# Performance work log

Measured on AMD Instinct MI355X. Metric: run time of the kernel, lower is better.

The kernel has to match this reference:

```python
import jax, jax.numpy as jnp
import numpy as np

CH = 256
NH = 8
HD = CH // NH  # 32


def setup_inputs() -> dict:
    key = jax.random.key(0)
    k1, k2, k3, k4 = jax.random.split(key, 4)
    x = jax.random.normal(k1, (2, CH, 16, 16, 16), dtype=jnp.float32)
    # 1x1x1 Conv3d weights == per-voxel linear maps over channels
    qkv_w = jax.random.normal(k2, (3 * CH, CH), dtype=jnp.float32) * (1.0 / np.sqrt(CH))
    proj_w = jax.random.normal(k3, (CH, CH), dtype=jnp.float32) * (1.0 / np.sqrt(CH))
    proj_b = jax.random.normal(k4, (CH,), dtype=jnp.float32) * 0.01
    return {"x": x, "qkv_w": qkv_w, "proj_w": proj_w, "proj_b": proj_b}


def reference(x, qkv_w, proj_w, proj_b):
    B, C, D, H, W = x.shape
    N = D * H * W
    nh, hd = NH, HD
    xf = x.reshape(B, C, N)  # [B, C, N]
    # qkv 1x1x1 conv: [B, 3C, N]
    qkv = jnp.einsum('oc,bcn->bon', qkv_w, xf)
    # split channel dim as (3, nh, hd), then arrange to [3, B, nh, N, hd]
    qkv = qkv.reshape(B, 3, nh, hd, N).transpose(1, 0, 2, 4, 3)
    q, k, v = qkv[0], qkv[1], qkv[2]
    scale = hd ** -0.5
    attn = jnp.einsum('bhqd,bhkd->bhqk', q, k) * scale  # [B, nh, N, N]
    attn = jax.nn.softmax(attn, axis=-1)
    # dropout is identity in eval mode
    out = jnp.einsum('bhqk,bhkd->bhqd', attn, v)  # [B, nh, N, hd]
    out = out.transpose(0, 1, 3, 2).reshape(B, C, D, H, W)
    out = jnp.einsum('oc,bcdhw->bodhw', proj_w, out) + proj_b[None, :, None, None, None]
    return out
```

## Files before the change

kernel.cpp:

```cpp
#include <hip/hip_runtime.h>
#include <hip/hip_bf16.h>

typedef __bf16 bf16;
typedef __bf16 bf16x8 __attribute__((ext_vector_type(8)));
typedef float f32x4 __attribute__((ext_vector_type(4)));
typedef float f32x16 __attribute__((ext_vector_type(16)));
typedef unsigned int u32x4 __attribute__((ext_vector_type(4)));

#define EXP2(x) __builtin_amdgcn_exp2f(x)

static __device__ __forceinline__ f32x4 mfma16(bf16x8 a, bf16x8 b, f32x4 c) {
    return __builtin_amdgcn_mfma_f32_16x16x32_bf16(a, b, c, 0, 0, 0);
}
static __device__ __forceinline__ f32x16 mfma32(bf16x8 a, bf16x8 b, f32x16 c) {
    return __builtin_amdgcn_mfma_f32_32x32x16_bf16(a, b, c, 0, 0, 0);
}
static __device__ __forceinline__ unsigned cvt_pk(float lo, float hi) {
    unsigned r;
    asm("v_cvt_pk_bf16_f32 %0, %1, %2" : "=v"(r) : "v"(lo), "v"(hi));
    return r;
}
static __device__ __forceinline__ void perm32swap(unsigned &a, unsigned &b) {
    asm("v_permlane32_swap_b32 %0, %1" : "+v"(a), "+v"(b));
}

__global__ __launch_bounds__(256) void prep_w_kernel(const float* __restrict__ qkv_w,
                                                     const float* __restrict__ proj_w,
                                                     bf16* __restrict__ wqkv,
                                                     bf16* __restrict__ wproj) {
    int idx = blockIdx.x * 256 + threadIdx.x;
    const float QSCALE = 0.17677669529663689f * 1.4426950408889634f;
    if (idx < 768 * 256) {
        float v = qkv_w[idx];
        if (idx < 256 * 256) v *= QSCALE;
        wqkv[idx] = (bf16)v;
    } else {
        int j = idx - 768 * 256;
        wproj[j] = (bf16)proj_w[j];
    }
}

__global__ __launch_bounds__(256) void transpose_x_kernel(const float* __restrict__ x,
                                                          bf16* __restrict__ xT) {
    __shared__ float tile[64][68];
    int b = blockIdx.z, cb = blockIdx.y * 64, nb = blockIdx.x * 64;
    int t = threadIdx.x;
    int j = t & 15, rc = t >> 4;
    const float* src = x + ((size_t)b * 256 + cb) * 4096 + nb;
#pragma unroll
    for (int i = 0; i < 4; i++) {
        f32x4 v = *(const f32x4*)(src + (size_t)(rc + i * 16) * 4096 + j * 4);
        *(f32x4*)&tile[rc + i * 16][j * 4] = v;
    }
    __syncthreads();
    int n = t >> 2;
    bf16* dst = xT + ((size_t)b * 4096 + nb + n) * 256 + cb;
#pragma unroll
    for (int i = 0; i < 2; i++) {
        int c0 = ((t & 3) + i * 4) * 8;
        bf16x8 v;
#pragma unroll
        for (int jj = 0; jj < 8; jj++) v[jj] = (bf16)tile[c0 + jj][n];
        *(bf16x8*)(dst + c0) = v;
    }
}

__global__ __launch_bounds__(256) void qkv_gemm_kernel(const bf16* __restrict__ xT,
                                                       const bf16* __restrict__ w,
                                                       bf16* __restrict__ Q,
                                                       bf16* __restrict__ Kp,
                                                       bf16* __restrict__ Vp) {
    int b = blockIdx.z;
    int nb = blockIdx.x * 64, ob = blockIdx.y * 128;
    int t = threadIdx.x, wid = t >> 6, lane = t & 63;
    int l15 = lane & 15, g = lane >> 4;
    int wr = wid >> 1, wc = wid & 1;
    const bf16* xrow = xT + ((size_t)b * 4096 + nb + wr * 32 + l15) * 256 + g * 8;
    const bf16* wrow = w + (size_t)(ob + wc * 64 + l15) * 256 + g * 8;
    f32x4 acc[2][4] = {};
    for (int k0 = 0; k0 < 256; k0 += 32) {
        bf16x8 a[2], bb[4];
#pragma unroll
        for (int rt = 0; rt < 2; rt++) a[rt] = *(const bf16x8*)(xrow + rt * 16 * 256 + k0);
#pragma unroll
        for (int cg = 0; cg < 4; cg++) bb[cg] = *(const bf16x8*)(wrow + cg * 16 * 256 + k0);
#pragma unroll
        for (int rt = 0; rt < 2; rt++)
#pragma unroll
            for (int cg = 0; cg < 4; cg++)
                acc[rt][cg] = mfma16(a[rt], bb[cg], acc[rt][cg]);
    }
#pragma unroll
    for (int rt = 0; rt < 2; rt++) {
#pragma unroll
        for (int cg = 0; cg < 4; cg++) {
            int o = ob + wc * 64 + cg * 16 + l15;
            int tsel = o >> 8;
            int h = (o >> 5) & 7;
            int d = o & 31;
            int n0 = nb + wr * 32 + rt * 16 + g * 4;
            size_t bhbase = ((size_t)b * 8 + h) * 131072;
            if (tsel == 0) {
#pragma unroll
                for (int i = 0; i < 4; i++)
                    Q[(((size_t)b * 8 + h) * 4096 + n0 + i) * 32 + d] = (bf16)acc[rt][cg][i];
            } else if (tsel == 1) {
                int kt = n0 >> 5;
                int which = d >> 4, hi2 = (d >> 3) & 1, j = d & 7;
                size_t base = bhbase + (size_t)(((kt * 2 + which) * 64 + hi2 * 32) * 8 + j);
#pragma unroll
                for (int i = 0; i < 4; i++) {
                    int r5 = (n0 + i) & 31;
                    Kp[base + r5 * 8] = (bf16)acc[rt][cg][i];
                }
            } else {
                int kt = n0 >> 5, kk0 = n0 & 31;
                int which = kk0 >> 4, hi2 = (kk0 >> 3) & 1, j0 = kk0 & 7;
                unsigned p0 = cvt_pk(acc[rt][cg][0], acc[rt][cg][1]);
                unsigned p1 = cvt_pk(acc[rt][cg][2], acc[rt][cg][3]);
                uint2 wv; wv.x = p0; wv.y = p1;
                *(uint2*)(Vp + bhbase + (size_t)(((kt * 2 + which) * 64 + hi2 * 32 + d) * 8 + j0)) = wv;
            }
        }
    }
}

#define PACK(stv, B, OUT) {                                  \
    unsigned _x01 = cvt_pk(stv[B + 0], stv[B + 1]);          \
    unsigned _x23 = cvt_pk(stv[B + 2], stv[B + 3]);          \
    unsigned _y01 = cvt_pk(stv[B + 4], stv[B + 5]);          \
    unsigned _y23 = cvt_pk(stv[B + 6], stv[B + 7]);          \
    perm32swap(_x01, _y01);                                  \
    perm32swap(_x23, _y23);                                  \
    u32x4 _w = {_x01, _x23, _y01, _y23};                     \
    OUT = __builtin_bit_cast(bf16x8, _w); }

__global__ __launch_bounds__(512, 6) void attn_kernel(const bf16* __restrict__ Q,
                                                      const bf16* __restrict__ Kp,
                                                      const bf16* __restrict__ Vp,
                                                      bf16* __restrict__ attT) {
    __shared__ __align__(16) float ldsO[3][2][64][20];
    __shared__ float ldsL[3][2][32];

    const int w = blockIdx.x;
    const int bh = (w & 7) + 8 * ((w >> 3) & 1);
    const int qblk = w >> 4;
    const int t = threadIdx.x;
    const int wid = t >> 6, lane = t & 63;
    const int z = wid >> 1, wq = wid & 1;
    const int l31 = lane & 31, hi = lane >> 5;
    const int q0 = qblk * 64 + wq * 32;

    const bf16* __restrict__ Qb = Q + (size_t)bh * 4096 * 32;
    const bf16* kptr = Kp + (size_t)bh * 131072 + (size_t)z * 32768 + lane * 8;
    const bf16* vptr = Vp + (size_t)bh * 131072 + (size_t)z * 32768 + lane * 8;

    bf16x8 qf0 = *(const bf16x8*)(Qb + (size_t)(q0 + l31) * 32 + hi * 8);
    bf16x8 qf1 = *(const bf16x8*)(Qb + (size_t)(q0 + l31) * 32 + 16 + hi * 8);

    const f32x16 ZERO16 = {};
    f32x16 o_acc = {};
    float lpart = 0.f;

    for (int it = 0; it < 32; ++it) {
        bf16x8 kf0 = *(const bf16x8*)(kptr);
        bf16x8 kf1 = *(const bf16x8*)(kptr + 512);
        bf16x8 vf0 = *(const bf16x8*)(vptr);
        bf16x8 vf1 = *(const bf16x8*)(vptr + 512);
        kptr += 1024; vptr += 1024;

        f32x16 st = mfma32(kf0, qf0, ZERO16);
        st = mfma32(kf1, qf1, st);

#pragma unroll
        for (int r = 0; r < 16; r++) st[r] = EXP2(st[r]);

        float s0 = 0.f, s1 = 0.f;
#pragma unroll
        for (int r = 0; r < 8; r++) { s0 += st[r]; s1 += st[r + 8]; }
        lpart += s0 + s1;

        bf16x8 pb0, pb1;
        PACK(st, 0, pb0);
        PACK(st, 8, pb1);

        __builtin_amdgcn_s_setprio(1);
        o_acc = mfma32(vf0, pb0, o_acc);
        o_acc = mfma32(vf1, pb1, o_acc);
        __builtin_amdgcn_s_setprio(0);
    }

    lpart += __shfl_xor(lpart, 32);

    if (z != 0) {
#pragma unroll
        for (int g = 0; g < 4; g++) {
            f32x4 wv = {o_acc[4 * g + 0], o_acc[4 * g + 1], o_acc[4 * g + 2], o_acc[4 * g + 3]};
            *(f32x4*)&ldsO[z - 1][wq][lane][4 * g] = wv;
        }
        if (hi == 0) ldsL[z - 1][wq][l31] = lpart;
    }
    __syncthreads();
    if (z == 0) {
        float lsum = lpart + ldsL[0][wq][l31] + ldsL[1][wq][l31] + ldsL[2][wq][l31];
        float inv = __builtin_amdgcn_rcpf(lsum);
        const int b = bh >> 3, h = bh & 7;
        bf16* orow = attT + ((size_t)b * 4096 + q0 + l31) * 256 + h * 32 + 4 * hi;
#pragma unroll
        for (int g = 0; g < 4; g++) {
            f32x4 p0 = *(const f32x4*)&ldsO[0][wq][lane][4 * g];
            f32x4 p1 = *(const f32x4*)&ldsO[1][wq][lane][4 * g];
            f32x4 p2 = *(const f32x4*)&ldsO[2][wq][lane][4 * g];
            float e0 = (o_acc[4 * g + 0] + p0[0] + p1[0] + p2[0]) * inv;
            float e1 = (o_acc[4 * g + 1] + p0[1] + p1[1] + p2[1]) * inv;
            float e2 = (o_acc[4 * g + 2] + p0[2] + p1[2] + p2[2]) * inv;
            float e3 = (o_acc[4 * g + 3] + p0[3] + p1[3] + p2[3]) * inv;
            uint2 wv;
            wv.x = cvt_pk(e0, e1);
            wv.y = cvt_pk(e2, e3);
            *(uint2*)(orow + 8 * g) = wv;
        }
    }
}

__global__ __launch_bounds__(256) void proj_gemm_kernel(const bf16* __restrict__ attT,
                                                        const bf16* __restrict__ w,
                                                        const float* __restrict__ bias,
                                                        float* __restrict__ out) {
    int b = blockIdx.z;
    int nb = blockIdx.x * 64, ob = blockIdx.y * 64;
    int t = threadIdx.x, wid = t >> 6, lane = t & 63;
    int l15 = lane & 15, g = lane >> 4;
    int wr = wid >> 1, wc = wid & 1;
    const bf16* arow = w + (size_t)(ob + wr * 32 + l15) * 256 + g * 8;
    const bf16* brow = attT + ((size_t)b * 4096 + nb + wc * 32 + l15) * 256 + g * 8;
    f32x4 acc[2][2] = {};
    for (int k0 = 0; k0 < 256; k0 += 32) {
        bf16x8 a[2], bb[2];
#pragma unroll
        for (int rt = 0; rt < 2; rt++) a[rt] = *(const bf16x8*)(arow + rt * 16 * 256 + k0);
#pragma unroll
        for (int cg = 0; cg < 2; cg++) bb[cg] = *(const bf16x8*)(brow + cg * 16 * 256 + k0);
#pragma unroll
        for (int rt = 0; rt < 2; rt++)
#pragma unroll
            for (int cg = 0; cg < 2; cg++)
                acc[rt][cg] = mfma16(a[rt], bb[cg], acc[rt][cg]);
    }
#pragma unroll
    for (int rt = 0; rt < 2; rt++)
#pragma unroll
        for (int cg = 0; cg < 2; cg++)
#pragma unroll
            for (int i = 0; i < 4; i++) {
                int o = ob + wr * 32 + rt * 16 + g * 4 + i;
                int n = nb + wc * 32 + cg * 16 + l15;
                out[((size_t)b * 256 + o) * 4096 + n] = acc[rt][cg][i] + bias[o];
            }
}

extern "C" void kernel_launch(void* const* d_in, const int* in_sizes, int n_in,
                              void* d_out, int out_size, void* d_ws, size_t ws_size,
                              hipStream_t stream) {
    const float* x      = (const float*)d_in[0];
    const float* qkv_w  = (const float*)d_in[1];
    const float* proj_w = (const float*)d_in[2];
    const float* proj_b = (const float*)d_in[3];
    float* out = (float*)d_out;

    char* ws = (char*)d_ws;
    bf16* xT    = (bf16*)(ws);
    bf16* wqkv  = (bf16*)(ws + 4194304);
    bf16* wproj = (bf16*)(ws + 4587520);
    bf16* Qb    = (bf16*)(ws + 4718592);
    bf16* Kp    = (bf16*)(ws + 8912896);
    bf16* Vp    = (bf16*)(ws + 13107200);
    bf16* attT  = (bf16*)(ws + 17301504);

    prep_w_kernel<<<1024, 256, 0, stream>>>(qkv_w, proj_w, wqkv, wproj);
    transpose_x_kernel<<<dim3(64, 4, 2), 256, 0, stream>>>(x, xT);
    qkv_gemm_kernel<<<dim3(64, 6, 2), 256, 0, stream>>>(xT, wqkv, Qb, Kp, Vp);
    attn_kernel<<<1024, 512, 0, stream>>>(Qb, Kp, Vp, attT);
    proj_gemm_kernel<<<dim3(64, 4, 2), 256, 0, stream>>>(attT, wproj, proj_b, out);
}
```

Measured before the change: 96.48 us.

## Share K/V loads across two query tiles per wave and pre-pack proj operands

The attention kernel now uses 256 threads, and each wave handles two 32-row query tiles. Each wave reuses the K and V fragments it loads for both tiles, halving global K/V traffic per query and doubling the work per wave. The attention output and the projection weight are now written in an MFMA-fragment-packed layout, so the projection GEMM uses 32x32x16 MFMAs with contiguous coalesced fragment loads. The trade-offs are more registers per wave (two accumulators) and the loss of the launch-bounds occupancy hint, which may reduce occupancy and latency hiding.

```diff
diff --git a/kernel.cpp b/kernel.cpp
--- a/kernel.cpp
+++ b/kernel.cpp
@@ -27,7 +27,7 @@
 __global__ __launch_bounds__(256) void prep_w_kernel(const float* __restrict__ qkv_w,
                                                      const float* __restrict__ proj_w,
                                                      bf16* __restrict__ wqkv,
-                                                     bf16* __restrict__ wproj) {
+                                                     bf16* __restrict__ Wp) {
     int idx = blockIdx.x * 256 + threadIdx.x;
     const float QSCALE = 0.17677669529663689f * 1.4426950408889634f;
     if (idx < 768 * 256) {
@@ -36,7 +36,10 @@
         wqkv[idx] = (bf16)v;
     } else {
         int j = idx - 768 * 256;
-        wproj[j] = (bf16)proj_w[j];
+        int o = j >> 8, c = j & 255;
+        int ot = o >> 5, l31 = o & 31;
+        int kc = c >> 4, hi = (c >> 3) & 1, jj = c & 7;
+        Wp[(size_t)(((ot * 16 + kc) * 64 + hi * 32 + l31) * 8 + jj)] = (bf16)proj_w[j];
     }
 }
 
@@ -135,10 +138,25 @@
     u32x4 _w = {_x01, _x23, _y01, _y23};                     \
     OUT = __builtin_bit_cast(bf16x8, _w); }
 
-__global__ __launch_bounds__(512, 6) void attn_kernel(const bf16* __restrict__ Q,
-                                                      const bf16* __restrict__ Kp,
-                                                      const bf16* __restrict__ Vp,
-                                                      bf16* __restrict__ attT) {
+#define PROC(ST, OACC, LP) {                                 \
+    _Pragma("unroll")                                        \
+    for (int r = 0; r < 16; r++) ST[r] = EXP2(ST[r]);        \
+    float _s0 = 0.f, _s1 = 0.f;                              \
+    _Pragma("unroll")                                        \
+    for (int r = 0; r < 8; r++) { _s0 += ST[r]; _s1 += ST[r + 8]; } \
+    LP += _s0 + _s1;                                         \
+    bf16x8 _pb0, _pb1;                                       \
+    PACK(ST, 0, _pb0);                                       \
+    PACK(ST, 8, _pb1);                                       \
+    __builtin_amdgcn_s_setprio(1);                           \
+    OACC = mfma32(vf0, _pb0, OACC);                          \
+    OACC = mfma32(vf1, _pb1, OACC);                          \
+    __builtin_amdgcn_s_setprio(0); }
+
+__global__ __launch_bounds__(256) void attn_kernel(const bf16* __restrict__ Q,
+                                                   const bf16* __restrict__ Kp,
+                                                   const bf16* __restrict__ Vp,
+                                                   bf16* __restrict__ attP) {
     __shared__ __align__(16) float ldsO[3][2][64][20];
     __shared__ float ldsL[3][2][32];
 
@@ -146,21 +164,22 @@
     const int bh = (w & 7) + 8 * ((w >> 3) & 1);
     const int qblk = w >> 4;
     const int t = threadIdx.x;
-    const int wid = t >> 6, lane = t & 63;
-    const int z = wid >> 1, wq = wid & 1;
+    const int z = t >> 6, lane = t & 63;
     const int l31 = lane & 31, hi = lane >> 5;
-    const int q0 = qblk * 64 + wq * 32;
+    const int q0 = qblk * 64;
 
     const bf16* __restrict__ Qb = Q + (size_t)bh * 4096 * 32;
     const bf16* kptr = Kp + (size_t)bh * 131072 + (size_t)z * 32768 + lane * 8;
     const bf16* vptr = Vp + (size_t)bh * 131072 + (size_t)z * 32768 + lane * 8;
 
-    bf16x8 qf0 = *(const bf16x8*)(Qb + (size_t)(q0 + l31) * 32 + hi * 8);
-    bf16x8 qf1 = *(const bf16x8*)(Qb + (size_t)(q0 + l31) * 32 + 16 + hi * 8);
+    bf16x8 qfA0 = *(const bf16x8*)(Qb + (size_t)(q0 + l31) * 32 + hi * 8);
+    bf16x8 qfA1 = *(const bf16x8*)(Qb + (size_t)(q0 + l31) * 32 + 16 + hi * 8);
+    bf16x8 qfB0 = *(const bf16x8*)(Qb + (size_t)(q0 + 32 + l31) * 32 + hi * 8);
+    bf16x8 qfB1 = *(const bf16x8*)(Qb + (size_t)(q0 + 32 + l31) * 32 + 16 + hi * 8);
 
     const f32x16 ZERO16 = {};
-    f32x16 o_acc = {};
-    float lpart = 0.f;
+    f32x16 oA = {}, oB = {};
+    float lA = 0.f, lB = 0.f;
 
     for (int it = 0; it < 32; ++it) {
         bf16x8 kf0 = *(const bf16x8*)(kptr);
@@ -169,94 +188,82 @@
         bf16x8 vf1 = *(const bf16x8*)(vptr + 512);
         kptr += 1024; vptr += 1024;
 
-        f32x16 st = mfma32(kf0, qf0, ZERO16);
-        st = mfma32(kf1, qf1, st);
-
-#pragma unroll
-        for (int r = 0; r < 16; r++) st[r] = EXP2(st[r]);
-
-        float s0 = 0.f, s1 = 0.f;
-#pragma unroll
-        for (int r = 0; r < 8; r++) { s0 += st[r]; s1 += st[r + 8]; }
-        lpart += s0 + s1;
-
-        bf16x8 pb0, pb1;
-        PACK(st, 0, pb0);
-        PACK(st, 8, pb1);
-
-        __builtin_amdgcn_s_setprio(1);
-        o_acc = mfma32(vf0, pb0, o_acc);
-        o_acc = mfma32(vf1, pb1, o_acc);
-        __builtin_amdgcn_s_setprio(0);
-    }
-
-    lpart += __shfl_xor(lpart, 32);
+        f32x16 st = mfma32(kf0, qfA0, ZERO16);
+        st = mfma32(kf1, qfA1, st);
+        PROC(st, oA, lA);
+        st = mfma32(kf0, qfB0, ZERO16);
+        st = mfma32(kf1, qfB1, st);
+        PROC(st, oB, lB);
+    }
+
+    lA += __shfl_xor(lA, 32);
+    lB += __shfl_xor(lB, 32);
 
     if (z != 0) {
 #pragma unroll
         for (int g = 0; g < 4; g++) {
-            f32x4 wv = {o_acc[4 * g + 0], o_acc[4 * g + 1], o_acc[4 * g + 2], o_acc[4 * g + 3]};
-            *(f32x4*)&ldsO[z - 1][wq][lane][4 * g] = wv;
+            *(f32x4*)&ldsO[z - 1][0][lane][4 * g] =
+                f32x4{oA[4 * g + 0], oA[4 * g + 1], oA[4 * g + 2], oA[4 * g + 3]};
+            *(f32x4*)&ldsO[z - 1][1][lane][4 * g] =
+                f32x4{oB[4 * g + 0], oB[4 * g + 1], oB[4 * g + 2], oB[4 * g + 3]};
         }
-        if (hi == 0) ldsL[z - 1][wq][l31] = lpart;
+        if (hi == 0) { ldsL[z - 1][0][l31] = lA; ldsL[z - 1][1][l31] = lB; }
     }
     __syncthreads();
     if (z == 0) {
-        float lsum = lpart + ldsL[0][wq][l31] + ldsL[1][wq][l31] + ldsL[2][wq][l31];
-        float inv = __builtin_amdgcn_rcpf(lsum);
         const int b = bh >> 3, h = bh & 7;
-        bf16* orow = attT + ((size_t)b * 4096 + q0 + l31) * 256 + h * 32 + 4 * hi;
-#pragma unroll
-        for (int g = 0; g < 4; g++) {
-            f32x4 p0 = *(const f32x4*)&ldsO[0][wq][lane][4 * g];
-            f32x4 p1 = *(const f32x4*)&ldsO[1][wq][lane][4 * g];
-            f32x4 p2 = *(const f32x4*)&ldsO[2][wq][lane][4 * g];
-            float e0 = (o_acc[4 * g + 0] + p0[0] + p1[0] + p2[0]) * inv;
-            float e1 = (o_acc[4 * g + 1] + p0[1] + p1[1] + p2[1]) * inv;
-            float e2 = (o_acc[4 * g + 2] + p0[2] + p1[2] + p2[2]) * inv;
-            float e3 = (o_acc[4 * g + 3] + p0[3] + p1[3] + p2[3]) * inv;
-            uint2 wv;
-            wv.x = cvt_pk(e0, e1);
-            wv.y = cvt_pk(e2, e3);
-            *(uint2*)(orow + 8 * g) = wv;
+#pragma unroll
+        for (int qg = 0; qg < 2; qg++) {
+            const f32x16& oo = qg ? oB : oA;
+            float lsum = (qg ? lB : lA) + ldsL[0][qg][l31] + ldsL[1][qg][l31] + ldsL[2][qg][l31];
+            float inv = __builtin_amdgcn_rcpf(lsum);
+            int nt = qblk * 2 + qg;
+            size_t base = (((size_t)b * 128 + nt) * 16) * 512;
+#pragma unroll
+            for (int g = 0; g < 4; g++) {
+                f32x4 p0 = *(const f32x4*)&ldsO[0][qg][lane][4 * g];
+                f32x4 p1 = *(const f32x4*)&ldsO[1][qg][lane][4 * g];
+                f32x4 p2 = *(const f32x4*)&ldsO[2][qg][lane][4 * g];
+                float e0 = (oo[4 * g + 0] + p0[0] + p1[0] + p2[0]) * inv;
+                float e1 = (oo[4 * g + 1] + p0[1] + p1[1] + p2[1]) * inv;
+                float e2 = (oo[4 * g + 2] + p0[2] + p1[2] + p2[2]) * inv;
+                float e3 = (oo[4 * g + 3] + p0[3] + p1[3] + p2[3]) * inv;
+                size_t addr = base + (size_t)(((h * 2 + (g >> 1)) * 64 + (g & 1) * 32 + l31) * 8 + 4 * hi);
+                uint2 wv;
+                wv.x = cvt_pk(e0, e1);
+                wv.y = cvt_pk(e2, e3);
+                *(uint2*)(attP + addr) = wv;
+            }
         }
     }
 }
 
-__global__ __launch_bounds__(256) void proj_gemm_kernel(const bf16* __restrict__ attT,
-                                                        const bf16* __restrict__ w,
+__global__ __launch_bounds__(256) void proj_gemm_kernel(const bf16* __restrict__ attP,
+                                                        const bf16* __restrict__ Wp,
                                                         const float* __restrict__ bias,
                                                         float* __restrict__ out) {
-    int b = blockIdx.z;
-    int nb = blockIdx.x * 64, ob = blockIdx.y * 64;
+    int bid = blockIdx.x;
+    int b = bid >> 8, rest = bid & 255;
+    int nt = rest >> 1, oh = rest & 1;
     int t = threadIdx.x, wid = t >> 6, lane = t & 63;
-    int l15 = lane & 15, g = lane >> 4;
-    int wr = wid >> 1, wc = wid & 1;
-    const bf16* arow = w + (size_t)(ob + wr * 32 + l15) * 256 + g * 8;
-    const bf16* brow = attT + ((size_t)b * 4096 + nb + wc * 32 + l15) * 256 + g * 8;
-    f32x4 acc[2][2] = {};
-    for (int k0 = 0; k0 < 256; k0 += 32) {
-        bf16x8 a[2], bb[2];
-#pragma unroll
-        for (int rt = 0; rt < 2; rt++) a[rt] = *(const bf16x8*)(arow + rt * 16 * 256 + k0);
-#pragma unroll
-        for (int cg = 0; cg < 2; cg++) bb[cg] = *(const bf16x8*)(brow + cg * 16 * 256 + k0);
-#pragma unroll
-        for (int rt = 0; rt < 2; rt++)
-#pragma unroll
-            for (int cg = 0; cg < 2; cg++)
-                acc[rt][cg] = mfma16(a[rt], bb[cg], acc[rt][cg]);
-    }
-#pragma unroll
-    for (int rt = 0; rt < 2; rt++)
-#pragma unroll
-        for (int cg = 0; cg < 2; cg++)
-#pragma unroll
-            for (int i = 0; i < 4; i++) {
-                int o = ob + wr * 32 + rt * 16 + g * 4 + i;
-                int n = nb + wc * 32 + cg * 16 + l15;
-                out[((size_t)b * 256 + o) * 4096 + n] = acc[rt][cg][i] + bias[o];
-            }
+    int l31 = lane & 31, hi = lane >> 5;
+    int ot = oh * 4 + wid;
+
+    const bf16* ap = Wp + (size_t)(ot * 16) * 512 + lane * 8;
+    const bf16* bp = attP + (((size_t)b * 128 + nt) * 16) * 512 + lane * 8;
+    f32x16 acc = {};
+#pragma unroll
+    for (int kc = 0; kc < 16; kc++) {
+        bf16x8 af = *(const bf16x8*)(ap + kc * 512);
+        bf16x8 bf = *(const bf16x8*)(bp + kc * 512);
+        acc = mfma32(af, bf, acc);
+    }
+    float* obase = out + ((size_t)b * 256 + ot * 32) * 4096 + nt * 32 + l31;
+#pragma unroll
+    for (int r = 0; r < 16; r++) {
+        int row = (r & 3) + 8 * (r >> 2) + 4 * hi;
+        obase[(size_t)row * 4096] = acc[r] + bias[ot * 32 + row];
+    }
 }
 
 extern "C" void kernel_launch(void* const* d_in, const int* in_sizes, int n_in,
@@ -271,15 +278,15 @@
     char* ws = (char*)d_ws;
     bf16* xT    = (bf16*)(ws);
     bf16* wqkv  = (bf16*)(ws + 4194304);
-    bf16* wproj = (bf16*)(ws + 4587520);
+    bf16* Wp    = (bf16*)(ws + 4587520);
     bf16* Qb    = (bf16*)(ws + 4718592);
     bf16* Kp    = (bf16*)(ws + 8912896);
     bf16* Vp    = (bf16*)(ws + 13107200);
-    bf16* attT  = (bf16*)(ws + 17301504);
-
-    prep_w_kernel<<<1024, 256, 0, stream>>>(qkv_w, proj_w, wqkv, wproj);
+    bf16* attP  = (bf16*)(ws + 17301504);
+
+    prep_w_kernel<<<1024, 256, 0, stream>>>(qkv_w, proj_w, wqkv, Wp);
     transpose_x_kernel<<<dim3(64, 4, 2), 256, 0, stream>>>(x, xT);
     qkv_gemm_kernel<<<dim3(64, 6, 2), 256, 0, stream>>>(xT, wqkv, Qb, Kp, Vp);
-    attn_kernel<<<1024, 512, 0, stream>>>(Qb, Kp, Vp, attT);
-    proj_gemm_kernel<<<dim3(64, 4, 2), 256, 0, stream>>>(attT, wproj, proj_b, out);
-}
+    attn_kernel<<<1024, 256, 0, stream>>>(Qb, Kp, Vp, attP);
+    proj_gemm_kernel<<<512, 256, 0, stream>>>(attP, Wp, proj_b, out);
+}
```

Result: slower. 99.74 us (+3.4%).
